# Performance work log

Hardware: AMD Instinct MI355X
Metric: run time of the kernel (lower is better)

Reference implementation:

```python
import jax, jax.numpy as jnp
import numpy as np

B, C, H, W = 64, 1, 1024, 1024
G, K, S = 64, 3, 2
HG0, HL = 512, 512
D_IN = K * G * G * C  # 12288


def setup_inputs() -> dict:
    key = jax.random.key(0)
    k1, k2, k3, k4, k5, k6 = jax.random.split(key, 6)
    x = jax.random.normal(k1, (B, C, H, W), dtype=jnp.float32)
    l_t_prev = jax.random.uniform(k2, (B, 2), dtype=jnp.float32, minval=-1.0, maxval=1.0)
    W1 = jax.random.normal(k3, (HG0, D_IN), dtype=jnp.float32) * 0.02
    W2 = jax.random.normal(k4, (HL, 2), dtype=jnp.float32) * 0.02
    W3 = jax.random.normal(k5, (HG0 + HL, HG0), dtype=jnp.float32) * 0.02
    W4 = jax.random.normal(k6, (HG0 + HL, HL), dtype=jnp.float32) * 0.02
    return {"x": x, "l_t_prev": l_t_prev, "W1": W1, "W2": W2, "W3": W3, "W4": W4}


def _extract_patch(x, coords, size):
    """Crop a size x size window per sample, centered at coords, zero-padded OOB,
    then avg-pool by factor size//G down to (B, C, G, G)."""
    r = size // G
    P = size // 2 + 1  # padding used by the torch code; makes every slice in-bounds
    xp = jnp.pad(x, ((0, 0), (0, 0), (P, P), (P, P)))
    sy = coords[:, 1] - size // 2 + P
    sx = coords[:, 0] - size // 2 + P

    def one(im, y0, x0):
        return jax.lax.dynamic_slice(im, (0, y0, x0), (C, size, size))

    p = jax.vmap(one)(xp, sy, sx)  # (B, C, size, size)
    if r > 1:
        p = p.reshape(B, C, G, r, G, r).mean(axis=(3, 5))  # avg_pool2d(kernel=r)
    return p


def _foveate(x, l):
    # denormalize: coords in [0, H], truncated to int
    coords = (0.5 * ((l + 1.0) * H)).astype(jnp.int32)  # (B, 2) as [x, y]
    patches = []
    size = G * S ** (K - 1)
    for _ in range(K):
        patches.append(_extract_patch(x, coords, size))  # (B, 1, G, G)
        size = size // S
    return jnp.concatenate(patches, axis=1)  # (B, K, G, G)


def reference(x, l_t_prev, W1, W2, W3, W4):
    phi = _foveate(x, l_t_prev)                      # (B, K, G, G)
    phi_flat = phi.reshape(phi.shape[0], -1)         # (B, K*G*G)
    h = jax.nn.leaky_relu(phi_flat @ W1.T)           # (B, HG0)
    l_out = jax.nn.leaky_relu(l_t_prev @ W2.T)       # computed but unused (as in source)
    what = h @ W3.T                                  # (B, HG0+HL)
    where = h @ W4.T                                 # fc4 applied to phi features (source quirk)
    g_t = jax.nn.leaky_relu(what + where)
    return g_t
```

## Files before the change

### kernel.cpp

```cpp
#include <hip/hip_runtime.h>
#include <hip/hip_bf16.h>

#define B_N 64
#define D_IN 12288
#define HG0 512
#define OUT_N 1024

#define KC1 16
#define DBLOCK1 768
#define DWAVE1 96

#define NFOV 3072
#define NW34 512

typedef __attribute__((ext_vector_type(8))) short bf16x8;
typedef __attribute__((ext_vector_type(4))) float f32x4;

static __device__ __forceinline__ short f2bf(float f) {
  __hip_bfloat16 h = __float2bfloat16(f);
  return *reinterpret_cast<short*>(&h);
}

__global__ __launch_bounds__(256) void prep_kernel(
    const float* __restrict__ x, const float* __restrict__ l,
    const float* __restrict__ W3, const float* __restrict__ W4,
    short* __restrict__ phi, short* __restrict__ w34) {
  int bx = blockIdx.x;
  if (bx >= NFOV) {
    int e = (bx - NFOV) * 1024 + threadIdx.x * 4;
    float4 a = *(const float4*)(W3 + e);
    float4 b = *(const float4*)(W4 + e);
    short4 o;
    o.x = f2bf(a.x + b.x); o.y = f2bf(a.y + b.y);
    o.z = f2bf(a.z + b.z); o.w = f2bf(a.w + b.w);
    *(short4*)(w34 + e) = o;
    return;
  }

  int idx = bx * 256 + threadIdx.x;
  int b = idx / D_IN;
  int d = idx - b * D_IN;
  int k = d >> 12;
  int rem = d & 4095;
  int gy = rem >> 6, gx = rem & 63;

  float lx = l[b * 2 + 0];
  float ly = l[b * 2 + 1];
  int cx = (int)(0.5f * ((lx + 1.0f) * 1024.0f));
  int cy = (int)(0.5f * ((ly + 1.0f) * 1024.0f));

  const float* xb = x + ((size_t)b << 20);
  float v;

  if (k == 0) {
    int y0 = cy - 128 + gy * 4;
    int x0 = cx - 128 + gx * 4;
    float s = 0.0f;
    #pragma unroll
    for (int dy = 0; dy < 4; ++dy) {
      int yy = y0 + dy;
      if ((unsigned)yy < 1024u) {
        const float* row = xb + ((size_t)yy << 10);
        #pragma unroll
        for (int dx = 0; dx < 4; ++dx) {
          int xx = x0 + dx;
          if ((unsigned)xx < 1024u) s += row[xx];
        }
      }
    }
    v = s * 0.0625f;
  } else if (k == 1) {
    int y0 = cy - 64 + gy * 2;
    int x0 = cx - 64 + gx * 2;
    float s = 0.0f;
    #pragma unroll
    for (int dy = 0; dy < 2; ++dy) {
      int yy = y0 + dy;
      if ((unsigned)yy < 1024u) {
        const float* row = xb + ((size_t)yy << 10);
        #pragma unroll
        for (int dx = 0; dx < 2; ++dx) {
          int xx = x0 + dx;
          if ((unsigned)xx < 1024u) s += row[xx];
        }
      }
    }
    v = s * 0.25f;
  } else {
    int yy = cy - 32 + gy;
    int xx = cx - 32 + gx;
    v = 0.0f;
    if ((unsigned)yy < 1024u && (unsigned)xx < 1024u) v = xb[((size_t)yy << 10) + xx];
  }
  phi[idx] = f2bf(v);
}

__global__ __launch_bounds__(512) void gemm1_kernel(
    const short* __restrict__ phi, const float* __restrict__ W1,
    float* __restrict__ partial1) {
  __shared__ float lds[8 * 16 * 64];
  int wave = threadIdx.x >> 6;
  int lane = threadIdx.x & 63;
  int lc = lane & 15;
  int kg = lane >> 4;
  int j0 = blockIdx.x * 16;
  int dbase = blockIdx.y * DBLOCK1 + wave * DWAVE1;

  f32x4 acc[4] = {{0,0,0,0},{0,0,0,0},{0,0,0,0},{0,0,0,0}};

  const float* wrow = W1 + (size_t)(j0 + lc) * D_IN + kg * 8;
  const short* prow = phi + kg * 8;

  #pragma unroll
  for (int ks = 0; ks < DWAVE1 / 32; ++ks) {
    int d0 = dbase + ks * 32;
    float4 wa = *(const float4*)(wrow + d0);
    float4 wb = *(const float4*)(wrow + d0 + 4);
    bf16x8 af;
    af[0] = f2bf(wa.x); af[1] = f2bf(wa.y); af[2] = f2bf(wa.z); af[3] = f2bf(wa.w);
    af[4] = f2bf(wb.x); af[5] = f2bf(wb.y); af[6] = f2bf(wb.z); af[7] = f2bf(wb.w);
    #pragma unroll
    for (int t = 0; t < 4; ++t) {
      bf16x8 bf = *(const bf16x8*)(prow + (size_t)(t * 16 + lc) * D_IN + d0);
      acc[t] = __builtin_amdgcn_mfma_f32_16x16x32_bf16(af, bf, acc[t], 0, 0, 0);
    }
  }

  #pragma unroll
  for (int t = 0; t < 4; ++t)
    #pragma unroll
    for (int r = 0; r < 4; ++r)
      lds[wave * 1024 + (kg * 4 + r) * 64 + t * 16 + lc] = acc[t][r];
  __syncthreads();

  float* pp = partial1 + (size_t)blockIdx.y * (HG0 * 64) + (size_t)j0 * 64;
  #pragma unroll
  for (int i = 0; i < 2; ++i) {
    int e = threadIdx.x + 512 * i;
    float s = 0.0f;
    #pragma unroll
    for (int w = 0; w < 8; ++w) s += lds[w * 1024 + e];
    pp[e] = s;
  }
}

__global__ __launch_bounds__(256) void reduce1_kernel(
    const float* __restrict__ partial1, short* __restrict__ h) {
  int idx = blockIdx.x * 256 + threadIdx.x;
  float s = 0.0f;
  #pragma unroll
  for (int kc = 0; kc < KC1; ++kc) s += partial1[(size_t)kc * (HG0 * 64) + idx];
  float v = (s >= 0.0f) ? s : 0.01f * s;
  int j = idx >> 6, b = idx & 63;
  h[(size_t)b * HG0 + j] = f2bf(v);
}

__global__ __launch_bounds__(256) void gemm2_kernel(
    const short* __restrict__ h, const short* __restrict__ w34,
    float* __restrict__ out) {
  __shared__ float lds[4 * 1024];
  int wave = threadIdx.x >> 6;
  int lane = threadIdx.x & 63;
  int lc = lane & 15;
  int kg = lane >> 4;
  int o0 = blockIdx.x * 16;
  int jbase = wave * 128;

  f32x4 acc[4] = {{0,0,0,0},{0,0,0,0},{0,0,0,0},{0,0,0,0}};

  #pragma unroll
  for (int ks = 0; ks < 4; ++ks) {
    int j0 = jbase + ks * 32;
    bf16x8 bf = *(const bf16x8*)(w34 + (size_t)(o0 + lc) * HG0 + j0 + kg * 8);
    #pragma unroll
    for (int t = 0; t < 4; ++t) {
      bf16x8 af = *(const bf16x8*)(h + (size_t)(t * 16 + lc) * HG0 + j0 + kg * 8);
      acc[t] = __builtin_amdgcn_mfma_f32_16x16x32_bf16(af, bf, acc[t], 0, 0, 0);
    }
  }

  #pragma unroll
  for (int t = 0; t < 4; ++t)
    #pragma unroll
    for (int r = 0; r < 4; ++r)
      lds[wave * 1024 + t * 256 + kg * 64 + r * 16 + lc] = acc[t][r];
  __syncthreads();

  #pragma unroll
  for (int i = 0; i < 4; ++i) {
    int e = threadIdx.x + 256 * i;
    float s = lds[e] + lds[1024 + e] + lds[2048 + e] + lds[3072 + e];
    float v = (s >= 0.0f) ? s : 0.01f * s;
    int b = ((e >> 8) << 4) + (((e >> 6) & 3) << 2) + ((e >> 4) & 3);
    out[(size_t)b * OUT_N + o0 + (e & 15)] = v;
  }
}

extern "C" void kernel_launch(void* const* d_in, const int* in_sizes, int n_in,
                              void* d_out, int out_size, void* d_ws, size_t ws_size,
                              hipStream_t stream) {
  const float* x  = (const float*)d_in[0];
  const float* l  = (const float*)d_in[1];
  const float* W1 = (const float*)d_in[2];
  const float* W3 = (const float*)d_in[4];
  const float* W4 = (const float*)d_in[5];
  float* out = (float*)d_out;

  char* ws = (char*)d_ws;
  short* phi      = (short*)(ws);
  float* partial1 = (float*)(ws + (2u << 20));
  short* h        = (short*)(ws + (6u << 20));
  short* w34      = (short*)(ws + (7u << 20));

  prep_kernel<<<dim3(NFOV + NW34), dim3(256), 0, stream>>>(x, l, W3, W4, phi, w34);
  gemm1_kernel<<<dim3(32, KC1), dim3(512), 0, stream>>>(phi, W1, partial1);
  reduce1_kernel<<<dim3((HG0 * 64) / 256), dim3(256), 0, stream>>>(partial1, h);
  gemm2_kernel<<<dim3(OUT_N / 16), dim3(256), 0, stream>>>(h, w34, out);
}
```

Before: 33.19 us.

## Pre-swizzle W1, phi, h and W34 into MFMA fragment order for coalesced loads

Adds a W1 conversion pass to the prep kernel that writes bf16 W1 in MFMA-fragment-tiled layout. phi, h and W3+W4 are also written in fragment order, so each lane's 16-byte load becomes contiguous across the wave. gemm1 drops from 512 to 256 threads per block, each wave covering 6 k-steps, and reads bf16 weights instead of converting fp32 in the inner loop. The cost is an extra full pass over W1 (25MB fp32 read plus 12.5MB bf16 write) on every call, which likely outweighs the gain from coalesced loads.

```diff
diff --git a/kernel.cpp b/kernel.cpp
--- a/kernel.cpp
+++ b/kernel.cpp
@@ -1,17 +1,17 @@
 #include <hip/hip_runtime.h>
 #include <hip/hip_bf16.h>
 
-#define B_N 64
 #define D_IN 12288
 #define HG0 512
 #define OUT_N 1024
 
 #define KC1 16
-#define DBLOCK1 768
-#define DWAVE1 96
+#define KSTEPS_BLK 24
+#define KSTEPS_WAVE 6
 
 #define NFOV 3072
-#define NW34 512
+#define NW1  3072
+#define NW34 256
 
 typedef __attribute__((ext_vector_type(8))) short bf16x8;
 typedef __attribute__((ext_vector_type(4))) float f32x4;
@@ -21,19 +21,44 @@
   return *reinterpret_cast<short*>(&h);
 }
 
+
 __global__ __launch_bounds__(256) void prep_kernel(
     const float* __restrict__ x, const float* __restrict__ l,
-    const float* __restrict__ W3, const float* __restrict__ W4,
-    short* __restrict__ phi, short* __restrict__ w34) {
+    const float* __restrict__ W1, const float* __restrict__ W3,
+    const float* __restrict__ W4,
+    short* __restrict__ phis, short* __restrict__ w1s,
+    short* __restrict__ w34s) {
   int bx = blockIdx.x;
+
+  if (bx >= NFOV + NW1) {
+    int g = (bx - NFOV - NW1) * 256 + threadIdx.x;
+    float4 a0 = *(const float4*)(W3 + (size_t)g * 8);
+    float4 a1 = *(const float4*)(W3 + (size_t)g * 8 + 4);
+    float4 b0 = *(const float4*)(W4 + (size_t)g * 8);
+    float4 b1 = *(const float4*)(W4 + (size_t)g * 8 + 4);
+    int r = g >> 6;
+    int c8 = g & 63;
+    int ot = r >> 4, lc = r & 15, ks = c8 >> 2, kg = c8 & 3;
+    bf16x8 o;
+    o[0] = f2bf(a0.x + b0.x); o[1] = f2bf(a0.y + b0.y);
+    o[2] = f2bf(a0.z + b0.z); o[3] = f2bf(a0.w + b0.w);
+    o[4] = f2bf(a1.x + b1.x); o[5] = f2bf(a1.y + b1.y);
+    o[6] = f2bf(a1.z + b1.z); o[7] = f2bf(a1.w + b1.w);
+    *(bf16x8*)(w34s + ((((size_t)ot * 16 + ks) * 64) + kg * 16 + lc) * 8) = o;
+    return;
+  }
+
   if (bx >= NFOV) {
-    int e = (bx - NFOV) * 1024 + threadIdx.x * 4;
-    float4 a = *(const float4*)(W3 + e);
-    float4 b = *(const float4*)(W4 + e);
-    short4 o;
-    o.x = f2bf(a.x + b.x); o.y = f2bf(a.y + b.y);
-    o.z = f2bf(a.z + b.z); o.w = f2bf(a.w + b.w);
-    *(short4*)(w34 + e) = o;
+    int g = (bx - NFOV) * 256 + threadIdx.x;
+    float4 a0 = *(const float4*)(W1 + (size_t)g * 8);
+    float4 a1 = *(const float4*)(W1 + (size_t)g * 8 + 4);
+    int r = g / 1536;
+    int c8 = g - r * 1536;
+    int jt = r >> 4, lc = r & 15, ks = c8 >> 2, kg = c8 & 3;
+    bf16x8 o;
+    o[0] = f2bf(a0.x); o[1] = f2bf(a0.y); o[2] = f2bf(a0.z); o[3] = f2bf(a0.w);
+    o[4] = f2bf(a1.x); o[5] = f2bf(a1.y); o[6] = f2bf(a1.z); o[7] = f2bf(a1.w);
+    *(bf16x8*)(w1s + ((((size_t)jt * 384 + ks) * 64) + kg * 16 + lc) * 8) = o;
     return;
   }
 
@@ -92,36 +117,32 @@
     v = 0.0f;
     if ((unsigned)yy < 1024u && (unsigned)xx < 1024u) v = xb[((size_t)yy << 10) + xx];
   }
-  phi[idx] = f2bf(v);
-}
-
-__global__ __launch_bounds__(512) void gemm1_kernel(
-    const short* __restrict__ phi, const float* __restrict__ W1,
+
+  int ks = d >> 5, kg = (d >> 3) & 3, e = d & 7, t = b >> 4, lcb = b & 15;
+  phis[(((size_t)ks * 4 + t) * 64 + kg * 16 + lcb) * 8 + e] = f2bf(v);
+}
+
+__global__ __launch_bounds__(256) void gemm1_kernel(
+    const short* __restrict__ phis, const short* __restrict__ w1s,
     float* __restrict__ partial1) {
-  __shared__ float lds[8 * 16 * 64];
+  __shared__ float lds[4 * 16 * 64];
   int wave = threadIdx.x >> 6;
   int lane = threadIdx.x & 63;
-  int lc = lane & 15;
-  int kg = lane >> 4;
-  int j0 = blockIdx.x * 16;
-  int dbase = blockIdx.y * DBLOCK1 + wave * DWAVE1;
+  int lc = lane & 15, kg = lane >> 4;
+  int jt = blockIdx.x;
+  int ksbase = blockIdx.y * KSTEPS_BLK + wave * KSTEPS_WAVE;
 
   f32x4 acc[4] = {{0,0,0,0},{0,0,0,0},{0,0,0,0},{0,0,0,0}};
 
-  const float* wrow = W1 + (size_t)(j0 + lc) * D_IN + kg * 8;
-  const short* prow = phi + kg * 8;
-
-  #pragma unroll
-  for (int ks = 0; ks < DWAVE1 / 32; ++ks) {
-    int d0 = dbase + ks * 32;
-    float4 wa = *(const float4*)(wrow + d0);
-    float4 wb = *(const float4*)(wrow + d0 + 4);
-    bf16x8 af;
-    af[0] = f2bf(wa.x); af[1] = f2bf(wa.y); af[2] = f2bf(wa.z); af[3] = f2bf(wa.w);
-    af[4] = f2bf(wb.x); af[5] = f2bf(wb.y); af[6] = f2bf(wb.z); af[7] = f2bf(wb.w);
+  const short* wbase = w1s + (((size_t)jt * 384 + ksbase) * 64 + lane) * 8;
+  const short* pbase = phis + ((size_t)ksbase * 4 * 64 + lane) * 8;
+
+  #pragma unroll
+  for (int s = 0; s < KSTEPS_WAVE; ++s) {
+    bf16x8 af = *(const bf16x8*)(wbase + (size_t)s * 512);
     #pragma unroll
     for (int t = 0; t < 4; ++t) {
-      bf16x8 bf = *(const bf16x8*)(prow + (size_t)(t * 16 + lc) * D_IN + d0);
+      bf16x8 bf = *(const bf16x8*)(pbase + ((size_t)s * 4 + t) * 512);
       acc[t] = __builtin_amdgcn_mfma_f32_16x16x32_bf16(af, bf, acc[t], 0, 0, 0);
     }
   }
@@ -133,49 +154,46 @@
       lds[wave * 1024 + (kg * 4 + r) * 64 + t * 16 + lc] = acc[t][r];
   __syncthreads();
 
-  float* pp = partial1 + (size_t)blockIdx.y * (HG0 * 64) + (size_t)j0 * 64;
-  #pragma unroll
-  for (int i = 0; i < 2; ++i) {
-    int e = threadIdx.x + 512 * i;
-    float s = 0.0f;
-    #pragma unroll
-    for (int w = 0; w < 8; ++w) s += lds[w * 1024 + e];
-    pp[e] = s;
+  float* pp = partial1 + (size_t)blockIdx.y * (HG0 * 64) + (size_t)jt * 1024;
+  #pragma unroll
+  for (int i = 0; i < 4; ++i) {
+    int e = threadIdx.x + 256 * i;
+    pp[e] = lds[e] + lds[1024 + e] + lds[2048 + e] + lds[3072 + e];
   }
 }
 
 __global__ __launch_bounds__(256) void reduce1_kernel(
-    const float* __restrict__ partial1, short* __restrict__ h) {
+    const float* __restrict__ partial1, short* __restrict__ hs) {
   int idx = blockIdx.x * 256 + threadIdx.x;
   float s = 0.0f;
   #pragma unroll
   for (int kc = 0; kc < KC1; ++kc) s += partial1[(size_t)kc * (HG0 * 64) + idx];
   float v = (s >= 0.0f) ? s : 0.01f * s;
   int j = idx >> 6, b = idx & 63;
-  h[(size_t)b * HG0 + j] = f2bf(v);
+  int ks = j >> 5, kg = (j >> 3) & 3, e = j & 7, t = b >> 4, lc = b & 15;
+  hs[(((size_t)ks * 4 + t) * 64 + kg * 16 + lc) * 8 + e] = f2bf(v);
 }
 
 __global__ __launch_bounds__(256) void gemm2_kernel(
-    const short* __restrict__ h, const short* __restrict__ w34,
+    const short* __restrict__ hs, const short* __restrict__ w34s,
     float* __restrict__ out) {
   __shared__ float lds[4 * 1024];
   int wave = threadIdx.x >> 6;
   int lane = threadIdx.x & 63;
-  int lc = lane & 15;
-  int kg = lane >> 4;
-  int o0 = blockIdx.x * 16;
-  int jbase = wave * 128;
+  int lc = lane & 15, kg = lane >> 4;
+  int ot = blockIdx.x;
+  int o0 = ot * 16;
 
   f32x4 acc[4] = {{0,0,0,0},{0,0,0,0},{0,0,0,0},{0,0,0,0}};
 
   #pragma unroll
-  for (int ks = 0; ks < 4; ++ks) {
-    int j0 = jbase + ks * 32;
-    bf16x8 bf = *(const bf16x8*)(w34 + (size_t)(o0 + lc) * HG0 + j0 + kg * 8);
+  for (int ksl = 0; ksl < 4; ++ksl) {
+    int kstep = wave * 4 + ksl;
+    bf16x8 bfr = *(const bf16x8*)(w34s + (((size_t)ot * 16 + kstep) * 64 + lane) * 8);
     #pragma unroll
     for (int t = 0; t < 4; ++t) {
-      bf16x8 af = *(const bf16x8*)(h + (size_t)(t * 16 + lc) * HG0 + j0 + kg * 8);
-      acc[t] = __builtin_amdgcn_mfma_f32_16x16x32_bf16(af, bf, acc[t], 0, 0, 0);
+      bf16x8 af = *(const bf16x8*)(hs + (((size_t)kstep * 4 + t) * 64 + lane) * 8);
+      acc[t] = __builtin_amdgcn_mfma_f32_16x16x32_bf16(af, bfr, acc[t], 0, 0, 0);
     }
   }
 
@@ -207,13 +225,15 @@
   float* out = (float*)d_out;
 
   char* ws = (char*)d_ws;
-  short* phi      = (short*)(ws);
-  float* partial1 = (float*)(ws + (2u << 20));
-  short* h        = (short*)(ws + (6u << 20));
-  short* w34      = (short*)(ws + (7u << 20));
-
-  prep_kernel<<<dim3(NFOV + NW34), dim3(256), 0, stream>>>(x, l, W3, W4, phi, w34);
-  gemm1_kernel<<<dim3(32, KC1), dim3(512), 0, stream>>>(phi, W1, partial1);
-  reduce1_kernel<<<dim3((HG0 * 64) / 256), dim3(256), 0, stream>>>(partial1, h);
-  gemm2_kernel<<<dim3(OUT_N / 16), dim3(256), 0, stream>>>(h, w34, out);
-}
+  short* phis     = (short*)(ws);
+  short* w1s      = (short*)(ws + (2u << 20));
+  float* partial1 = (float*)(ws + (16u << 20));
+  short* hs       = (short*)(ws + (19u << 20));
+  short* w34s     = (short*)(ws + (20u << 20));
+
+  prep_kernel<<<dim3(NFOV + NW1 + NW34), dim3(256), 0, stream>>>(
+      x, l, W1, W3, W4, phis, w1s, w34s);
+  gemm1_kernel<<<dim3(32, KC1), dim3(256), 0, stream>>>(phis, w1s, partial1);
+  reduce1_kernel<<<dim3((HG0 * 64) / 256), dim3(256), 0, stream>>>(partial1, hs);
+  gemm2_kernel<<<dim3(OUT_N / 16), dim3(256), 0, stream>>>(hs, w34s, out);
+}
```

Result: slower. 36.15 us (+8.9%).
